# Kernel optimization log

Measured on AMD Instinct MI355X. Metric: run time of the kernel, lower is better.

Reference implementation:

```python
import jax, jax.numpy as jnp
import numpy as np

KERNEL_SIZE = 3
STRIDE = 1

def setup_inputs() -> dict:
    key = jax.random.key(0)
    kx, kw, kb = jax.random.split(key, 3)
    B, C_in, L = 32, 64, 16384
    C_out = 64
    x = jax.random.normal(kx, (B, C_in, L), dtype=jnp.float32)
    # original uses torch.rand (uniform [0,1)) for params
    weight = jax.random.uniform(kw, (C_out, C_in, KERNEL_SIZE), dtype=jnp.float32)
    bias = jax.random.uniform(kb, (C_out,), dtype=jnp.float32)
    return {"x": x, "weight": weight, "bias": bias}

def reference(x, weight, bias):
    # x: (B, C_in, L), weight: (C_out, C_in, K) -> out: (B, C_out, L_out)
    out = jax.lax.conv_general_dilated(
        x, weight,
        window_strides=(STRIDE,),
        padding="VALID",
        dimension_numbers=("NCH", "OIH", "NCH"),
    )
    return out + bias[None, :, None]
```

## Files before the change

### kernel.cpp

```cpp
#include <hip/hip_runtime.h>


typedef __bf16 bf16x8 __attribute__((ext_vector_type(8)));
typedef unsigned short ushort8 __attribute__((ext_vector_type(8)));
typedef float f32x16 __attribute__((ext_vector_type(16)));

#define C_IN 64
#define C_OUT 64
#define L_IN 16384
#define L_OUT 16382
#define NT 256
#define PW 200

__device__ __forceinline__ unsigned short f2bf(float f) {
  unsigned u = __builtin_bit_cast(unsigned, f);
  return (unsigned short)((u + 0x7FFFu + ((u >> 16) & 1u)) >> 16);
}

__global__ __launch_bounds__(256, 4) void conv1d_mfma(
    const float* __restrict__ x, const float* __restrict__ w,
    const float* __restrict__ bias, float* __restrict__ out) {
  __shared__ __align__(16) unsigned short wl[C_OUT * PW];
  __shared__ float bias_s[C_OUT];

  const int t = threadIdx.x;
  const int bx = blockIdx.x;
  const int b = bx >> 6;
  const int tile = bx & 63;
  const int l0 = tile * NT;

  for (int i = t; i < C_OUT * 192; i += 256) {
    int co = i / 192;
    int r = i - co * 192;
    int ci = r / 3;
    int kk = r - ci * 3;
    wl[co * PW + kk * 64 + ci] = f2bf(w[i]);
  }
  if (t < C_OUT) bias_s[t] = bias[t];
  __syncthreads();

  const int lane = t & 63;
  const int wv = t >> 6;
  const int half = lane >> 5;
  const int ln = lane & 31;
  const int kh = half * 8;
  const int n0 = wv * 64 + ln;
  const int l_a = l0 + n0;

  const float* xb = x + (size_t)b * (C_IN * L_IN);

  f32x16 acc00 = {}, acc01 = {}, acc10 = {}, acc11 = {};

#pragma unroll
  for (int s = 0; s < 12; ++s) {
    bf16x8 a0 = *(const bf16x8*)&wl[ln * PW + s * 16 + kh];
    bf16x8 a1 = *(const bf16x8*)&wl[(32 + ln) * PW + s * 16 + kh];

    int tt = s * 16 + kh;
    int kk = tt >> 6;
    int ci0 = tt & 63;
    int p0 = min(l_a + kk, L_IN - 1);
    int p1 = min(l_a + 32 + kk, L_IN - 1);
    int base = ci0 * L_IN;
    ushort8 b0u, b1u;
#pragma unroll
    for (int jj = 0; jj < 8; ++jj) {
      b0u[jj] = f2bf(xb[base + jj * L_IN + p0]);
      b1u[jj] = f2bf(xb[base + jj * L_IN + p1]);
    }
    bf16x8 b0 = __builtin_bit_cast(bf16x8, b0u);
    bf16x8 b1 = __builtin_bit_cast(bf16x8, b1u);
    acc00 = __builtin_amdgcn_mfma_f32_32x32x16_bf16(a0, b0, acc00, 0, 0, 0);
    acc01 = __builtin_amdgcn_mfma_f32_32x32x16_bf16(a0, b1, acc01, 0, 0, 0);
    acc10 = __builtin_amdgcn_mfma_f32_32x32x16_bf16(a1, b0, acc10, 0, 0, 0);
    acc11 = __builtin_amdgcn_mfma_f32_32x32x16_bf16(a1, b1, acc11, 0, 0, 0);
  }

  const int l_base = l0 + wv * 64 + ln;
  const bool full = (l0 + NT <= L_OUT);
  if (full) {
#pragma unroll
    for (int mt = 0; mt < 2; ++mt) {
#pragma unroll
      for (int r = 0; r < 16; ++r) {
        int co = mt * 32 + 4 * half + (r & 3) + 8 * (r >> 2);
        float bv = bias_s[co];
        size_t row = ((size_t)b * C_OUT + co) * (size_t)L_OUT;
        float v0 = (mt == 0 ? acc00[r] : acc10[r]) + bv;
        float v1 = (mt == 0 ? acc01[r] : acc11[r]) + bv;
        out[row + l_base] = v0;
        out[row + l_base + 32] = v1;
      }
    }
  } else {
#pragma unroll
    for (int mt = 0; mt < 2; ++mt) {
#pragma unroll
      for (int r = 0; r < 16; ++r) {
        int co = mt * 32 + 4 * half + (r & 3) + 8 * (r >> 2);
        float bv = bias_s[co];
        size_t row = ((size_t)b * C_OUT + co) * (size_t)L_OUT;
        float v0 = (mt == 0 ? acc00[r] : acc10[r]) + bv;
        float v1 = (mt == 0 ? acc01[r] : acc11[r]) + bv;
        if (l_base < L_OUT) out[row + l_base] = v0;
        if (l_base + 32 < L_OUT) out[row + l_base + 32] = v1;
      }
    }
  }
}

extern "C" void kernel_launch(void* const* d_in, const int* in_sizes, int n_in,
                              void* d_out, int out_size, void* d_ws, size_t ws_size,
                              hipStream_t stream) {
  const float* x = (const float*)d_in[0];
  const float* w = (const float*)d_in[1];
  const float* bias = (const float*)d_in[2];
  float* out = (float*)d_out;
  conv1d_mfma<<<dim3(32 * 64), dim3(256), 0, stream>>>(x, w, bias, out);
}
```

Baseline: 283.9 us.

## Precompute bf16 weights in a prep kernel and read them from global memory

```diff
diff --git a/kernel.cpp b/kernel.cpp
--- a/kernel.cpp
+++ b/kernel.cpp
@@ -2,7 +2,6 @@
 
 
 typedef __bf16 bf16x8 __attribute__((ext_vector_type(8)));
-typedef unsigned short ushort8 __attribute__((ext_vector_type(8)));
 typedef float f32x16 __attribute__((ext_vector_type(16)));
 
 #define C_IN 64
@@ -10,34 +9,26 @@
 #define L_IN 16384
 #define L_OUT 16382
 #define NT 256
-#define PW 200
 
-__device__ __forceinline__ unsigned short f2bf(float f) {
-  unsigned u = __builtin_bit_cast(unsigned, f);
-  return (unsigned short)((u + 0x7FFFu + ((u >> 16) & 1u)) >> 16);
+__global__ void prep_w(const float* __restrict__ w, __bf16* __restrict__ wg) {
+  int i = blockIdx.x * 256 + threadIdx.x;
+  if (i < C_OUT * 192) {
+    int co = i / 192;
+    int r = i - co * 192;
+    int ci = r / 3;
+    int kk = r - ci * 3;
+    wg[co * 192 + kk * 64 + ci] = (__bf16)w[i];
+  }
 }
 
 __global__ __launch_bounds__(256, 4) void conv1d_mfma(
-    const float* __restrict__ x, const float* __restrict__ w,
+    const float* __restrict__ x, const __bf16* __restrict__ wg,
     const float* __restrict__ bias, float* __restrict__ out) {
-  __shared__ __align__(16) unsigned short wl[C_OUT * PW];
-  __shared__ float bias_s[C_OUT];
-
   const int t = threadIdx.x;
   const int bx = blockIdx.x;
   const int b = bx >> 6;
   const int tile = bx & 63;
   const int l0 = tile * NT;
-
-  for (int i = t; i < C_OUT * 192; i += 256) {
-    int co = i / 192;
-    int r = i - co * 192;
-    int ci = r / 3;
-    int kk = r - ci * 3;
-    wl[co * PW + kk * 64 + ci] = f2bf(w[i]);
-  }
-  if (t < C_OUT) bias_s[t] = bias[t];
-  __syncthreads();
 
   const int lane = t & 63;
   const int wv = t >> 6;
@@ -52,28 +43,28 @@
   f32x16 acc00 = {}, acc01 = {}, acc10 = {}, acc11 = {};
 
 #pragma unroll
-  for (int s = 0; s < 12; ++s) {
-    bf16x8 a0 = *(const bf16x8*)&wl[ln * PW + s * 16 + kh];
-    bf16x8 a1 = *(const bf16x8*)&wl[(32 + ln) * PW + s * 16 + kh];
+  for (int g = 0; g < 4; ++g) {
+#pragma unroll
+    for (int kk = 0; kk < 3; ++kk) {
+      const int s = kk * 4 + g;
+      bf16x8 a0 = *(const bf16x8*)&wg[ln * 192 + s * 16 + kh];
+      bf16x8 a1 = *(const bf16x8*)&wg[(32 + ln) * 192 + s * 16 + kh];
 
-    int tt = s * 16 + kh;
-    int kk = tt >> 6;
-    int ci0 = tt & 63;
-    int p0 = min(l_a + kk, L_IN - 1);
-    int p1 = min(l_a + 32 + kk, L_IN - 1);
-    int base = ci0 * L_IN;
-    ushort8 b0u, b1u;
+      const int ci0 = 16 * g + kh;
+      const int p0 = min(l_a + kk, L_IN - 1);
+      const int p1 = min(l_a + 32 + kk, L_IN - 1);
+      const int base = ci0 * L_IN;
+      bf16x8 b0, b1;
 #pragma unroll
-    for (int jj = 0; jj < 8; ++jj) {
-      b0u[jj] = f2bf(xb[base + jj * L_IN + p0]);
-      b1u[jj] = f2bf(xb[base + jj * L_IN + p1]);
+      for (int jj = 0; jj < 8; ++jj) {
+        b0[jj] = (__bf16)xb[base + jj * L_IN + p0];
+        b1[jj] = (__bf16)xb[base + jj * L_IN + p1];
+      }
+      acc00 = __builtin_amdgcn_mfma_f32_32x32x16_bf16(a0, b0, acc00, 0, 0, 0);
+      acc01 = __builtin_amdgcn_mfma_f32_32x32x16_bf16(a0, b1, acc01, 0, 0, 0);
+      acc10 = __builtin_amdgcn_mfma_f32_32x32x16_bf16(a1, b0, acc10, 0, 0, 0);
+      acc11 = __builtin_amdgcn_mfma_f32_32x32x16_bf16(a1, b1, acc11, 0, 0, 0);
     }
-    bf16x8 b0 = __builtin_bit_cast(bf16x8, b0u);
-    bf16x8 b1 = __builtin_bit_cast(bf16x8, b1u);
-    acc00 = __builtin_amdgcn_mfma_f32_32x32x16_bf16(a0, b0, acc00, 0, 0, 0);
-    acc01 = __builtin_amdgcn_mfma_f32_32x32x16_bf16(a0, b1, acc01, 0, 0, 0);
-    acc10 = __builtin_amdgcn_mfma_f32_32x32x16_bf16(a1, b0, acc10, 0, 0, 0);
-    acc11 = __builtin_amdgcn_mfma_f32_32x32x16_bf16(a1, b1, acc11, 0, 0, 0);
   }
 
   const int l_base = l0 + wv * 64 + ln;
@@ -84,7 +75,7 @@
 #pragma unroll
       for (int r = 0; r < 16; ++r) {
         int co = mt * 32 + 4 * half + (r & 3) + 8 * (r >> 2);
-        float bv = bias_s[co];
+        float bv = bias[co];
         size_t row = ((size_t)b * C_OUT + co) * (size_t)L_OUT;
         float v0 = (mt == 0 ? acc00[r] : acc10[r]) + bv;
         float v1 = (mt == 0 ? acc01[r] : acc11[r]) + bv;
@@ -98,7 +89,7 @@
 #pragma unroll
       for (int r = 0; r < 16; ++r) {
         int co = mt * 32 + 4 * half + (r & 3) + 8 * (r >> 2);
-        float bv = bias_s[co];
+        float bv = bias[co];
         size_t row = ((size_t)b * C_OUT + co) * (size_t)L_OUT;
         float v0 = (mt == 0 ? acc00[r] : acc10[r]) + bv;
         float v1 = (mt == 0 ? acc01[r] : acc11[r]) + bv;
@@ -116,5 +107,8 @@
   const float* w = (const float*)d_in[1];
   const float* bias = (const float*)d_in[2];
   float* out = (float*)d_out;
-  conv1d_mfma<<<dim3(32 * 64), dim3(256), 0, stream>>>(x, w, bias, out);
+  __bf16* wg = (__bf16*)d_ws;
+
+  prep_w<<<dim3(48), dim3(256), 0, stream>>>(w, wg);
+  conv1d_mfma<<<dim3(32 * 64), dim3(256), 0, stream>>>(x, wg, bias, out);
 }
```

New measurement: 304.8 us. 7.4% more time.
